# Performance work log

Measured on AMD Instinct MI355X. Metric: run time of the kernel, lower is better.

## Reference

```python
import jax, jax.numpy as jnp
import numpy as np

N = 50000      # nodes
E = 800000     # edges (avg in-degree 16)
IN_DIM = 128
OUT_DIM = 64
LEAKY_SLOPE = 0.01  # torch F.leaky_relu default


def setup_inputs() -> dict:
    key = jax.random.key(0)
    ks = jax.random.split(key, 7)
    h = jax.random.normal(ks[0], (N, IN_DIM), dtype=jnp.float32)
    r_h = jax.random.normal(ks[1], (E, OUT_DIM), dtype=jnp.float32)
    edge_src = jax.random.randint(ks[2], (E,), 0, N, dtype=jnp.int32)
    edge_dst = jax.random.randint(ks[3], (E,), 0, N, dtype=jnp.int32)
    # learned params (xavier-ish scaling)
    W_fc = jax.random.normal(ks[4], (OUT_DIM, IN_DIM), dtype=jnp.float32) * (1.0 / np.sqrt(IN_DIM))
    attn_w = jax.random.normal(ks[5], (1, 3 * OUT_DIM), dtype=jnp.float32) * 0.1
    loop_weight = jax.random.normal(ks[6], (OUT_DIM, OUT_DIM), dtype=jnp.float32) * (1.0 / np.sqrt(OUT_DIM))
    return {"h": h, "r_h": r_h, "W_fc": W_fc, "attn_w": attn_w,
            "loop_weight": loop_weight, "edge_src": edge_src, "edge_dst": edge_dst}


def reference(h, r_h, W_fc, attn_w, loop_weight, edge_src, edge_dst):
    # z = fc(h)   [N, OUT_DIM]
    z = h @ W_fc.T
    z_src = z[edge_src]          # [E, OUT_DIM]
    z_dst = z[edge_dst]          # [E, OUT_DIM]
    # attn_fc(cat([z_src, z_dst, r_h])) expressed without materializing the concat
    w1 = attn_w[0, :OUT_DIM]
    w2 = attn_w[0, OUT_DIM:2 * OUT_DIM]
    w3 = attn_w[0, 2 * OUT_DIM:]
    a = z_src @ w1 + z_dst @ w2 + r_h @ w3            # [E]
    e = jax.nn.leaky_relu(a, LEAKY_SLOPE)
    # segment softmax over incoming edges of each destination node
    seg_max = jax.ops.segment_max(e, edge_dst, num_segments=N)  # -inf for deg-0 (never gathered)
    e_exp = jnp.exp(e - jax.lax.stop_gradient(seg_max)[edge_dst])
    denom = jax.ops.segment_sum(e_exp, edge_dst, num_segments=N)
    alpha = e_exp / denom[edge_dst]                   # [E]
    # weighted scatter-sum of source features
    agg = jax.ops.segment_sum(alpha[:, None] * z_src, edge_dst, num_segments=N)  # [N, OUT_DIM]
    # DGL only runs reduce_func (incl. self-loop matmul) on nodes with in-edges
    deg = jax.ops.segment_sum(jnp.ones((E,), jnp.float32), edge_dst, num_segments=N)
    h_out = jnp.where(deg[:, None] > 0, agg + z @ loop_weight, 0.0)
    return jax.nn.relu(h_out)
```

## Files before the change

### kernel.cpp

```cpp
#include <hip/hip_runtime.h>
#include <hip/hip_bf16.h>

#define NN 50000
#define EE 800000
#define IND 128
#define OUTD 64
#define NB 49
#define PA_BLOCKS 782
#define DEG_BLOCKS 391
#define RH_BLOCKS 6250

__global__ __launch_bounds__(256, 1) void k_front(
    const float* __restrict__ h, const float* __restrict__ W,
    const float* __restrict__ attn, const int* __restrict__ edst,
    const float* __restrict__ r_h,
    __hip_bfloat16* __restrict__ zb, float* __restrict__ s1,
    float* __restrict__ s2, int* __restrict__ deg, int* __restrict__ rank,
    float* __restrict__ d3) {
  const int tid = threadIdx.x;
  if (blockIdx.x >= PA_BLOCKS + DEG_BLOCKS) {
    const int base4 = (blockIdx.x - (PA_BLOCKS + DEG_BLOCKS)) * 2048 + tid;
    const int sub = tid & 15;
    const float4 wv = reinterpret_cast<const float4*>(attn + 2 * OUTD)[sub];
    float4 rv[8];
#pragma unroll
    for (int j = 0; j < 8; ++j)
      rv[j] = reinterpret_cast<const float4*>(r_h)[base4 + j * 256];
    float d[8];
#pragma unroll
    for (int j = 0; j < 8; ++j)
      d[j] = rv[j].x * wv.x + rv[j].y * wv.y + rv[j].z * wv.z + rv[j].w * wv.w;
#pragma unroll
    for (int m = 1; m <= 8; m <<= 1) {
#pragma unroll
      for (int j = 0; j < 8; ++j) d[j] += __shfl_xor(d[j], m, 64);
    }
    if (sub == 0) {
      const int row0 = base4 >> 4;
#pragma unroll
      for (int j = 0; j < 8; ++j) d3[row0 + 16 * j] = d[j];
    }
    return;
  }
  if (blockIdx.x >= PA_BLOCKS) {
    const int base = (blockIdx.x - PA_BLOCKS) * 2048 + tid;
#pragma unroll
    for (int j = 0; j < 8; ++j) {
      int e = base + j * 256;
      if (e < EE) rank[e] = atomicAdd(&deg[edst[e]], 1);
    }
    return;
  }
  __shared__ float Wl[64 * 129];
#pragma unroll
  for (int j = 0; j < 8; ++j) {
    int i4 = tid + j * 256;
    const float4 v = reinterpret_cast<const float4*>(W)[i4];
    int i = i4 * 4;
    int col = i >> 7, k = i & 127;
    float* p = &Wl[col * 129 + k];
    p[0] = v.x; p[1] = v.y; p[2] = v.z; p[3] = v.w;
  }
  __syncthreads();
  const int lane = tid & 63;
  const int wid = tid >> 6;
  float Wreg[128];
#pragma unroll
  for (int k = 0; k < 128; ++k) Wreg[k] = Wl[lane * 129 + k];
  const float w1v = attn[lane];
  const float w2v = attn[64 + lane];
  const int base = blockIdx.x * 64 + wid * 16;
  int rmax = NN - base;
  rmax = rmax > 16 ? 16 : (rmax < 0 ? 0 : rmax);
  for (int i = 0; i < rmax; ++i) {
    int r = base + i;
    const float* hr = h + (size_t)r * IND;
    float h0 = hr[lane];
    float h1 = hr[64 + lane];
    float a0 = 0.f, a1 = 0.f, a2 = 0.f, a3 = 0.f;
#pragma unroll
    for (int k = 0; k < 16; ++k) {
      a0 = fmaf(__uint_as_float(__builtin_amdgcn_readlane(__float_as_uint(h0), 4 * k)),     Wreg[4 * k], a0);
      a1 = fmaf(__uint_as_float(__builtin_amdgcn_readlane(__float_as_uint(h0), 4 * k + 1)), Wreg[4 * k + 1], a1);
      a2 = fmaf(__uint_as_float(__builtin_amdgcn_readlane(__float_as_uint(h0), 4 * k + 2)), Wreg[4 * k + 2], a2);
      a3 = fmaf(__uint_as_float(__builtin_amdgcn_readlane(__float_as_uint(h0), 4 * k + 3)), Wreg[4 * k + 3], a3);
    }
#pragma unroll
    for (int k = 0; k < 16; ++k) {
      a0 = fmaf(__uint_as_float(__builtin_amdgcn_readlane(__float_as_uint(h1), 4 * k)),     Wreg[64 + 4 * k], a0);
      a1 = fmaf(__uint_as_float(__builtin_amdgcn_readlane(__float_as_uint(h1), 4 * k + 1)), Wreg[64 + 4 * k + 1], a1);
      a2 = fmaf(__uint_as_float(__builtin_amdgcn_readlane(__float_as_uint(h1), 4 * k + 2)), Wreg[64 + 4 * k + 2], a2);
      a3 = fmaf(__uint_as_float(__builtin_amdgcn_readlane(__float_as_uint(h1), 4 * k + 3)), Wreg[64 + 4 * k + 3], a3);
    }
    float acc = (a0 + a1) + (a2 + a3);
    zb[(size_t)r * OUTD + lane] = __float2bfloat16(acc);
    float p = acc * w1v, q = acc * w2v;
#pragma unroll
    for (int m = 32; m >= 1; m >>= 1) {
      p += __shfl_xor(p, m, 64);
      q += __shfl_xor(q, m, 64);
    }
    if (lane == 0) { s1[r] = p; s2[r] = q; }
  }
}

__global__ __launch_bounds__(1024) void k_scan1(
    const int* __restrict__ deg, int* __restrict__ offL,
    int* __restrict__ blocksum) {
  __shared__ int wsum[16];
  __shared__ int woff[17];
  const int tid = threadIdx.x;
  const int gid = blockIdx.x * 1024 + tid;
  const int lane = tid & 63, wid = tid >> 6;
  int v = (gid < NN) ? deg[gid] : 0;
  int incl = v;
#pragma unroll
  for (int o = 1; o < 64; o <<= 1) {
    int t = __shfl_up(incl, o, 64);
    if (lane >= o) incl += t;
  }
  if (lane == 63) wsum[wid] = incl;
  __syncthreads();
  if (wid == 0 && lane < 16) {
    int s = wsum[lane];
    int si = s;
#pragma unroll
    for (int o = 1; o < 16; o <<= 1) {
      int t = __shfl_up(si, o, 64);
      if (lane >= o) si += t;
    }
    woff[lane] = si - s;
    if (lane == 15) woff[16] = si;
  }
  __syncthreads();
  if (gid < NN) offL[gid] = woff[wid] + incl - v;
  if (tid == 0) blocksum[blockIdx.x] = woff[16];
}

__global__ __launch_bounds__(256) void k_scatter(
    const int* __restrict__ esrc, const int* __restrict__ edst,
    const float* __restrict__ d3, const float* __restrict__ s1,
    const float* __restrict__ s2, const int* __restrict__ rank,
    const int* __restrict__ offL, const int* __restrict__ bsum,
    int2* __restrict__ pairs) {
  __shared__ int boffs[NB];
  if (threadIdx.x < 64) {
    int l = threadIdx.x;
    int v = (l < NB) ? bsum[l] : 0;
    int incl = v;
#pragma unroll
    for (int o = 1; o < 64; o <<= 1) {
      int t = __shfl_up(incl, o, 64);
      if (l >= o) incl += t;
    }
    if (l < NB) boffs[l] = incl - v;
  }
  __syncthreads();
  const int t = blockIdx.x * 256 + threadIdx.x;
  if (t >= EE / 4) return;
  const int4 s4 = reinterpret_cast<const int4*>(esrc)[t];
  const int4 dd4 = reinterpret_cast<const int4*>(edst)[t];
  const float4 d34 = reinterpret_cast<const float4*>(d3)[t];
  const int4 rk4 = reinterpret_cast<const int4*>(rank)[t];
  float v1x = s1[s4.x], v1y = s1[s4.y], v1z = s1[s4.z], v1w = s1[s4.w];
  float v2x = s2[dd4.x], v2y = s2[dd4.y], v2z = s2[dd4.z], v2w = s2[dd4.w];
  int oLx = offL[dd4.x], oLy = offL[dd4.y], oLz = offL[dd4.z], oLw = offL[dd4.w];
  int bx = boffs[dd4.x >> 10], by = boffs[dd4.y >> 10];
  int bz = boffs[dd4.z >> 10], bw = boffs[dd4.w >> 10];
  float ax = v1x + v2x + d34.x, ay = v1y + v2y + d34.y;
  float az = v1z + v2z + d34.z, aw = v1w + v2w + d34.w;
  float ex = __expf(ax > 0.f ? ax : 0.01f * ax);
  float ey = __expf(ay > 0.f ? ay : 0.01f * ay);
  float ez = __expf(az > 0.f ? az : 0.01f * az);
  float ew = __expf(aw > 0.f ? aw : 0.01f * aw);
  pairs[bx + oLx + rk4.x] = make_int2(s4.x, __float_as_int(ex));
  pairs[by + oLy + rk4.y] = make_int2(s4.y, __float_as_int(ey));
  pairs[bz + oLz + rk4.z] = make_int2(s4.z, __float_as_int(ez));
  pairs[bw + oLw + rk4.w] = make_int2(s4.w, __float_as_int(ew));
}

__global__ __launch_bounds__(256) void k_agg(
    const __hip_bfloat16* __restrict__ zb, const int2* __restrict__ pairs,
    const int* __restrict__ offL, const int* __restrict__ bsum,
    const int* __restrict__ deg, const float* __restrict__ LW,
    float* __restrict__ out) {
  __shared__ int boffs[NB];
  if (threadIdx.x < 64) {
    int l = threadIdx.x;
    int v = (l < NB) ? bsum[l] : 0;
    int incl = v;
#pragma unroll
    for (int o = 1; o < 64; o <<= 1) {
      int t = __shfl_up(incl, o, 64);
      if (l >= o) incl += t;
    }
    if (l < NB) boffs[l] = incl - v;
  }
  __syncthreads();
  const int lane = threadIdx.x & 63, wid = threadIdx.x >> 6;
  const int slot = lane >> 4, sub = lane & 15;
  float4 LWreg[16];
#pragma unroll
  for (int kl = 0; kl < 16; ++kl)
    LWreg[kl] = reinterpret_cast<const float4*>(LW)[(slot * 16 + kl) * 16 + sub];
  const int r = blockIdx.x * 4 + wid;
  const int cnt = deg[r];
  const int2* pp = pairs + (boffs[r >> 10] + offL[r]);
  float4 acc = make_float4(0.f, 0.f, 0.f, 0.f);
  float wsum = 0.f;
  for (int i = 0; i < cnt; i += 16) {
    int2 p[4];
    float w[4];
#pragma unroll
    for (int j = 0; j < 4; ++j) {
      int e = i + j * 4 + slot;
      bool v = e < cnt;
      p[j] = pp[v ? e : 0];
      w[j] = v ? __int_as_float(p[j].y) : 0.f;
    }
#pragma unroll
    for (int j = 0; j < 4; ++j) {
      ushort4 uz = reinterpret_cast<const ushort4*>(zb)[(size_t)p[j].x * 16 + sub];
      acc.x = fmaf(w[j], __uint_as_float((unsigned)uz.x << 16), acc.x);
      acc.y = fmaf(w[j], __uint_as_float((unsigned)uz.y << 16), acc.y);
      acc.z = fmaf(w[j], __uint_as_float((unsigned)uz.z << 16), acc.z);
      acc.w = fmaf(w[j], __uint_as_float((unsigned)uz.w << 16), acc.w);
      wsum += w[j];
    }
  }
  float4 lacc = make_float4(0.f, 0.f, 0.f, 0.f);
#pragma unroll
  for (int j = 0; j < 4; ++j) {
    ushort4 uz = reinterpret_cast<const ushort4*>(zb)[(size_t)r * 16 + slot * 4 + j];
    float zk[4] = {__uint_as_float((unsigned)uz.x << 16),
                   __uint_as_float((unsigned)uz.y << 16),
                   __uint_as_float((unsigned)uz.z << 16),
                   __uint_as_float((unsigned)uz.w << 16)};
#pragma unroll
    for (int c = 0; c < 4; ++c) {
      float4 lw = LWreg[4 * j + c];
      lacc.x = fmaf(zk[c], lw.x, lacc.x);
      lacc.y = fmaf(zk[c], lw.y, lacc.y);
      lacc.z = fmaf(zk[c], lw.z, lacc.z);
      lacc.w = fmaf(zk[c], lw.w, lacc.w);
    }
  }
  wsum += __shfl_xor(wsum, 16, 64);
  wsum += __shfl_xor(wsum, 32, 64);
  float inv = (cnt > 0) ? 1.f / wsum : 0.f;
  float4 t;
  t.x = fmaf(acc.x, inv, lacc.x);
  t.y = fmaf(acc.y, inv, lacc.y);
  t.z = fmaf(acc.z, inv, lacc.z);
  t.w = fmaf(acc.w, inv, lacc.w);
  t.x += __shfl_xor(t.x, 16, 64); t.x += __shfl_xor(t.x, 32, 64);
  t.y += __shfl_xor(t.y, 16, 64); t.y += __shfl_xor(t.y, 32, 64);
  t.z += __shfl_xor(t.z, 16, 64); t.z += __shfl_xor(t.z, 32, 64);
  t.w += __shfl_xor(t.w, 16, 64); t.w += __shfl_xor(t.w, 32, 64);
  if (slot == 0) {
    float4 res;
    res.x = (cnt > 0 && t.x > 0.f) ? t.x : 0.f;
    res.y = (cnt > 0 && t.y > 0.f) ? t.y : 0.f;
    res.z = (cnt > 0 && t.z > 0.f) ? t.z : 0.f;
    res.w = (cnt > 0 && t.w > 0.f) ? t.w : 0.f;
    reinterpret_cast<float4*>(out)[(size_t)r * 16 + sub] = res;
  }
}

extern "C" void kernel_launch(void* const* d_in, const int* in_sizes, int n_in,
                              void* d_out, int out_size, void* d_ws, size_t ws_size,
                              hipStream_t stream) {
  const float* h    = (const float*)d_in[0];
  const float* r_h  = (const float*)d_in[1];
  const float* W_fc = (const float*)d_in[2];
  const float* attn = (const float*)d_in[3];
  const float* LW   = (const float*)d_in[4];
  const int* esrc   = (const int*)d_in[5];
  const int* edst   = (const int*)d_in[6];
  float* out = (float*)d_out;

  char* ws = (char*)d_ws;
  __hip_bfloat16* zb = (__hip_bfloat16*)(ws);
  int2*  pairs = (int2*)(ws + 6400000);
  int*   rank  = (int*)(ws + 12800000);
  float* d3    = (float*)(ws + 16000000);
  float* s1    = (float*)(ws + 19200000);
  float* s2    = (float*)(ws + 19400000);
  int*   deg   = (int*)(ws + 19600000);
  int*   offL  = (int*)(ws + 19800000);
  int*   bsum  = (int*)(ws + 20000000);

  hipMemsetAsync(deg, 0, (size_t)NN * sizeof(int), stream);

  k_front<<<PA_BLOCKS + DEG_BLOCKS + RH_BLOCKS, 256, 0, stream>>>(
      h, W_fc, attn, edst, r_h, zb, s1, s2, deg, rank, d3);
  k_scan1<<<NB, 1024, 0, stream>>>(deg, offL, bsum);
  k_scatter<<<(EE / 4 + 255) / 256, 256, 0, stream>>>(
      esrc, edst, d3, s1, s2, rank, offL, bsum, pairs);
  k_agg<<<NN / 4, 256, 0, stream>>>(zb, pairs, offL, bsum, deg, LW, out);
}
```

Before: 424.6 us.

## Replace readlane row GEMV with shared-memory 4x4 register-tiled GEMM in front kernel

The projection z = h @ W^T in the front kernel moves from a per-wave, row-by-row readlane GEMV (W held in 128 registers per lane) to a block-tiled GEMM. It stages 16-wide K slices of h and W in shared memory, and each thread computes a 4x4 output tile. Writes become packed bf16x4 and the attention dot reductions shrink to 16-lane shuffles. Dropping the min-occupancy-1 launch bound and the 128-register W copy is meant to raise occupancy and cut serialized readlane work. The cost is extra syncthreads and LDS traffic per K-step.

```diff
diff --git a/kernel.cpp b/kernel.cpp
--- a/kernel.cpp
+++ b/kernel.cpp
@@ -10,13 +10,15 @@
 #define DEG_BLOCKS 391
 #define RH_BLOCKS 6250
 
-__global__ __launch_bounds__(256, 1) void k_front(
+__global__ __launch_bounds__(256) void k_front(
     const float* __restrict__ h, const float* __restrict__ W,
     const float* __restrict__ attn, const int* __restrict__ edst,
     const float* __restrict__ r_h,
     __hip_bfloat16* __restrict__ zb, float* __restrict__ s1,
     float* __restrict__ s2, int* __restrict__ deg, int* __restrict__ rank,
     float* __restrict__ d3) {
+  __shared__ float sA[16][68];
+  __shared__ float sB[16][68];
   const int tid = threadIdx.x;
   if (blockIdx.x >= PA_BLOCKS + DEG_BLOCKS) {
     const int base4 = (blockIdx.x - (PA_BLOCKS + DEG_BLOCKS)) * 2048 + tid;
@@ -51,56 +53,65 @@
     }
     return;
   }
-  __shared__ float Wl[64 * 129];
-#pragma unroll
-  for (int j = 0; j < 8; ++j) {
-    int i4 = tid + j * 256;
-    const float4 v = reinterpret_cast<const float4*>(W)[i4];
-    int i = i4 * 4;
-    int col = i >> 7, k = i & 127;
-    float* p = &Wl[col * 129 + k];
-    p[0] = v.x; p[1] = v.y; p[2] = v.z; p[3] = v.w;
-  }
-  __syncthreads();
-  const int lane = tid & 63;
-  const int wid = tid >> 6;
-  float Wreg[128];
-#pragma unroll
-  for (int k = 0; k < 128; ++k) Wreg[k] = Wl[lane * 129 + k];
-  const float w1v = attn[lane];
-  const float w2v = attn[64 + lane];
-  const int base = blockIdx.x * 64 + wid * 16;
-  int rmax = NN - base;
-  rmax = rmax > 16 ? 16 : (rmax < 0 ? 0 : rmax);
-  for (int i = 0; i < rmax; ++i) {
-    int r = base + i;
-    const float* hr = h + (size_t)r * IND;
-    float h0 = hr[lane];
-    float h1 = hr[64 + lane];
-    float a0 = 0.f, a1 = 0.f, a2 = 0.f, a3 = 0.f;
+  const int base = blockIdx.x * 64;
+  const int lrow = tid >> 2;
+  const int lk4 = (tid & 3) * 4;
+  const int tr = tid >> 4;
+  const int tc = tid & 15;
+  int grow = base + lrow;
+  if (grow >= NN) grow = NN - 1;
+  const float* hrow = h + (size_t)grow * IND;
+  const float* wrow = W + lrow * IND;
+  float acc[4][4] = {};
+  for (int c = 0; c < 8; ++c) {
+    const int k0 = c * 16;
+    const float4 av = *reinterpret_cast<const float4*>(hrow + k0 + lk4);
+    const float4 bv = *reinterpret_cast<const float4*>(wrow + k0 + lk4);
+    sA[lk4 + 0][lrow] = av.x; sA[lk4 + 1][lrow] = av.y;
+    sA[lk4 + 2][lrow] = av.z; sA[lk4 + 3][lrow] = av.w;
+    sB[lk4 + 0][lrow] = bv.x; sB[lk4 + 1][lrow] = bv.y;
+    sB[lk4 + 2][lrow] = bv.z; sB[lk4 + 3][lrow] = bv.w;
+    __syncthreads();
 #pragma unroll
     for (int k = 0; k < 16; ++k) {
-      a0 = fmaf(__uint_as_float(__builtin_amdgcn_readlane(__float_as_uint(h0), 4 * k)),     Wreg[4 * k], a0);
-      a1 = fmaf(__uint_as_float(__builtin_amdgcn_readlane(__float_as_uint(h0), 4 * k + 1)), Wreg[4 * k + 1], a1);
-      a2 = fmaf(__uint_as_float(__builtin_amdgcn_readlane(__float_as_uint(h0), 4 * k + 2)), Wreg[4 * k + 2], a2);
-      a3 = fmaf(__uint_as_float(__builtin_amdgcn_readlane(__float_as_uint(h0), 4 * k + 3)), Wreg[4 * k + 3], a3);
-    }
-#pragma unroll
-    for (int k = 0; k < 16; ++k) {
-      a0 = fmaf(__uint_as_float(__builtin_amdgcn_readlane(__float_as_uint(h1), 4 * k)),     Wreg[64 + 4 * k], a0);
-      a1 = fmaf(__uint_as_float(__builtin_amdgcn_readlane(__float_as_uint(h1), 4 * k + 1)), Wreg[64 + 4 * k + 1], a1);
-      a2 = fmaf(__uint_as_float(__builtin_amdgcn_readlane(__float_as_uint(h1), 4 * k + 2)), Wreg[64 + 4 * k + 2], a2);
-      a3 = fmaf(__uint_as_float(__builtin_amdgcn_readlane(__float_as_uint(h1), 4 * k + 3)), Wreg[64 + 4 * k + 3], a3);
-    }
-    float acc = (a0 + a1) + (a2 + a3);
-    zb[(size_t)r * OUTD + lane] = __float2bfloat16(acc);
-    float p = acc * w1v, q = acc * w2v;
-#pragma unroll
-    for (int m = 32; m >= 1; m >>= 1) {
+      const float4 a = *reinterpret_cast<const float4*>(&sA[k][tr * 4]);
+      const float4 b = *reinterpret_cast<const float4*>(&sB[k][tc * 4]);
+      acc[0][0] = fmaf(a.x, b.x, acc[0][0]); acc[0][1] = fmaf(a.x, b.y, acc[0][1]);
+      acc[0][2] = fmaf(a.x, b.z, acc[0][2]); acc[0][3] = fmaf(a.x, b.w, acc[0][3]);
+      acc[1][0] = fmaf(a.y, b.x, acc[1][0]); acc[1][1] = fmaf(a.y, b.y, acc[1][1]);
+      acc[1][2] = fmaf(a.y, b.z, acc[1][2]); acc[1][3] = fmaf(a.y, b.w, acc[1][3]);
+      acc[2][0] = fmaf(a.z, b.x, acc[2][0]); acc[2][1] = fmaf(a.z, b.y, acc[2][1]);
+      acc[2][2] = fmaf(a.z, b.z, acc[2][2]); acc[2][3] = fmaf(a.z, b.w, acc[2][3]);
+      acc[3][0] = fmaf(a.w, b.x, acc[3][0]); acc[3][1] = fmaf(a.w, b.y, acc[3][1]);
+      acc[3][2] = fmaf(a.w, b.z, acc[3][2]); acc[3][3] = fmaf(a.w, b.w, acc[3][3]);
+    }
+    __syncthreads();
+  }
+  const float4 w1v = *reinterpret_cast<const float4*>(attn + tc * 4);
+  const float4 w2v = *reinterpret_cast<const float4*>(attn + OUTD + tc * 4);
+#pragma unroll
+  for (int i = 0; i < 4; ++i) {
+    const int r = base + tr * 4 + i;
+    const bool valid = r < NN;
+    const float zx = acc[i][0], zy = acc[i][1], zz = acc[i][2], zw = acc[i][3];
+    float p = zx * w1v.x + zy * w1v.y + zz * w1v.z + zw * w1v.w;
+    float q = zx * w2v.x + zy * w2v.y + zz * w2v.z + zw * w2v.w;
+#pragma unroll
+    for (int m = 1; m <= 8; m <<= 1) {
       p += __shfl_xor(p, m, 64);
       q += __shfl_xor(q, m, 64);
     }
-    if (lane == 0) { s1[r] = p; s2[r] = q; }
+    if (valid) {
+      __hip_bfloat16 b0 = __float2bfloat16(zx), b1 = __float2bfloat16(zy);
+      __hip_bfloat16 b2 = __float2bfloat16(zz), b3 = __float2bfloat16(zw);
+      ushort4 u;
+      u.x = reinterpret_cast<unsigned short&>(b0);
+      u.y = reinterpret_cast<unsigned short&>(b1);
+      u.z = reinterpret_cast<unsigned short&>(b2);
+      u.w = reinterpret_cast<unsigned short&>(b3);
+      reinterpret_cast<ushort4*>(zb)[(size_t)r * 16 + tc] = u;
+      if (tc == 0) { s1[r] = p; s2[r] = q; }
+    }
   }
 }
 
```

After: 397.4 us. -6.4%, faster.
